# Kernel optimization log

Hardware: AMD Instinct MI355X
Metric: run time of the kernel (lower is better)

Reference implementation:

```python
import jax, jax.numpy as jnp
import numpy as np
import math

FREQ_SEL = [(0, 0), (0, 1), (1, 0), (1, 1)]


def _dct_mat(N):
    # Faithful replica of the module's custom dct1d matrix:
    # A[i, j] = cos(pi * j * (2i + 1) / (2N)) * sqrt(2/N), with row 0 scaled by sqrt(0.5).
    i = np.arange(N, dtype=np.float32)[:, None]
    j = np.arange(N, dtype=np.float32)[None, :]
    A = np.cos(math.pi * j * (2.0 * i + 1.0) / (2.0 * N)) * math.sqrt(2.0 / N)
    A[0] *= math.sqrt(0.5)
    return jnp.asarray(A, dtype=jnp.float32)


def _basis(H, W):
    # coeff(u, v) = sum_{h,w} A_H[u, h] * A_W[v, w] * x[h, w]
    # (both DCT stages in the torch code contract against ROWS of A)
    A_H = _dct_mat(H)
    A_W = _dct_mat(W)
    planes = [A_H[u][:, None] * A_W[v][None, :] for (u, v) in FREQ_SEL]
    return jnp.stack(planes, axis=0)  # [F, H, W]


def setup_inputs() -> dict:
    key = jax.random.key(0)
    k1, k2, k3 = jax.random.split(key, 3)
    B, C, H, W = 32, 256, 64, 64
    hidden = C // 4
    x = jax.random.normal(k1, (B, C, H, W), dtype=jnp.float32)
    w1 = jax.random.normal(k2, (hidden, C), dtype=jnp.float32) * (1.0 / math.sqrt(C))
    w2 = jax.random.normal(k3, (C, hidden), dtype=jnp.float32) * (1.0 / math.sqrt(hidden))
    return {"x": x, "w1": w1, "w2": w2}


def reference(x, w1, w2):
    B, C, H, W = x.shape
    basis = _basis(H, W)                      # [F, H, W]
    spectral = jnp.einsum('bchw,fhw->bcf', x, basis)   # [B, C, F]
    y = jnp.einsum('bcf,hc->bhf', spectral, w1)        # fc1 (1x1 conv1d)
    y = jax.nn.relu(y)
    y = jnp.einsum('bhf,ch->bcf', y, w2)               # fc2
    gate = jax.nn.sigmoid(jnp.mean(y, axis=-1))        # [B, C]
    return x * gate[:, :, None, None]
```

## Files before the change

### kernel.cpp

```cpp
#include <hip/hip_runtime.h>

#define B_  32
#define C_  256
#define HID 64
#define H_  64
#define W_  64
#define HW  4096
#define F_  4

typedef float fvec4 __attribute__((ext_vector_type(4)));

__global__ __launch_bounds__(256) void spectral_kernel(
        const float* __restrict__ x, float* __restrict__ spectral) {
    const int plane = blockIdx.x;
    const int t = threadIdx.x;

    __shared__ float r0[W_], r1[W_];
    if (t < 64) {
        float fh = (float)t;
        r0[t] = cosf(fh * 0.02454369260617026f) * 0.125f;
        r1[t] = cosf(fh * 0.07363107781851077f) * 0.17677669529663689f;
    }
    __syncthreads();

    const float4* xv = (const float4*)(x + (size_t)plane * HW);
    float f0 = 0.f, f1 = 0.f, f2 = 0.f, f3 = 0.f;

    #pragma unroll
    for (int q = 0; q < 4; ++q) {
        int v = q * 256 + t;
        float4 d = xv[v];
        int h  = v >> 4;
        int wb = (v & 15) << 2;
        float r0h = r0[h], r1h = r1[h];
        float e, t0, t1;
        e = d.x; t0 = e * r0[wb+0]; t1 = e * r1[wb+0];
        f0 += r0h*t0; f1 += r0h*t1; f2 += r1h*t0; f3 += r1h*t1;
        e = d.y; t0 = e * r0[wb+1]; t1 = e * r1[wb+1];
        f0 += r0h*t0; f1 += r0h*t1; f2 += r1h*t0; f3 += r1h*t1;
        e = d.z; t0 = e * r0[wb+2]; t1 = e * r1[wb+2];
        f0 += r0h*t0; f1 += r0h*t1; f2 += r1h*t0; f3 += r1h*t1;
        e = d.w; t0 = e * r0[wb+3]; t1 = e * r1[wb+3];
        f0 += r0h*t0; f1 += r0h*t1; f2 += r1h*t0; f3 += r1h*t1;
    }

    #pragma unroll
    for (int off = 32; off >= 1; off >>= 1) {
        f0 += __shfl_down(f0, off);
        f1 += __shfl_down(f1, off);
        f2 += __shfl_down(f2, off);
        f3 += __shfl_down(f3, off);
    }
    __shared__ float part[4][F_];
    int wave = t >> 6, lane = t & 63;
    if (lane == 0) { part[wave][0]=f0; part[wave][1]=f1; part[wave][2]=f2; part[wave][3]=f3; }
    __syncthreads();
    if (t == 0) {
        float4 s;
        s.x = part[0][0]+part[1][0]+part[2][0]+part[3][0];
        s.y = part[0][1]+part[1][1]+part[2][1]+part[3][1];
        s.z = part[0][2]+part[1][2]+part[2][2]+part[3][2];
        s.w = part[0][3]+part[1][3]+part[2][3]+part[3][3];
        ((float4*)spectral)[plane] = s;
    }
}

__global__ __launch_bounds__(256) void gate_kernel(
        const float* __restrict__ spectral, const float* __restrict__ w1,
        const float* __restrict__ w2, float* __restrict__ gate) {
    const int b = blockIdx.x;
    const int t = threadIdx.x;

    __shared__ float s[C_][F_];
    __shared__ float y[HID][F_];

    ((float4*)&s[0][0])[t] = ((const float4*)(spectral + (size_t)b * C_ * F_))[t];
    __syncthreads();

    {
        int h = t >> 2, f = t & 3;
        const float* w1r = w1 + h * C_;
        float a0 = 0.f, a1 = 0.f, a2 = 0.f, a3 = 0.f;
        #pragma unroll 4
        for (int c = 0; c < C_; c += 4) {
            a0 += s[c+0][f] * w1r[c+0];
            a1 += s[c+1][f] * w1r[c+1];
            a2 += s[c+2][f] * w1r[c+2];
            a3 += s[c+3][f] * w1r[c+3];
        }
        y[h][f] = fmaxf((a0 + a1) + (a2 + a3), 0.f);
    }
    __syncthreads();

    {
        int c = t;
        const float* w2r = w2 + c * HID;
        float a0=0.f, a1=0.f, a2=0.f, a3=0.f;
        #pragma unroll 8
        for (int h = 0; h < HID; ++h) {
            float wv = w2r[h];
            a0 += y[h][0]*wv; a1 += y[h][1]*wv; a2 += y[h][2]*wv; a3 += y[h][3]*wv;
        }
        float m = (a0 + a1 + a2 + a3) * 0.25f;
        gate[b * C_ + c] = 1.f / (1.f + __expf(-m) );
    }
}

__global__ __launch_bounds__(256) void scale_kernel(
        const float* __restrict__ x, const float* __restrict__ gate,
        float* __restrict__ out, long long n4) {
    long long i = (long long)blockIdx.x * 256 + threadIdx.x;
    const long long stride = (long long)gridDim.x * 256;
    for (; i < n4; i += stride) {
        fvec4 v = ((const fvec4*)x)[i];
        float g = gate[i >> 10];
        v *= g;
        __builtin_nontemporal_store(v, ((fvec4*)out) + i);
    }
}

extern "C" void kernel_launch(void* const* d_in, const int* in_sizes, int n_in,
                              void* d_out, int out_size, void* d_ws, size_t ws_size,
                              hipStream_t stream) {
    const float* x  = (const float*)d_in[0];
    const float* w1 = (const float*)d_in[1];
    const float* w2 = (const float*)d_in[2];
    float* out = (float*)d_out;

    float* spectral = (float*)d_ws;
    float* gate     = (float*)d_ws + (size_t)B_ * C_ * F_;

    spectral_kernel<<<B_ * C_, 256, 0, stream>>>(x, spectral);
    gate_kernel<<<B_, 256, 0, stream>>>(spectral, w1, w2, gate);

    const long long n4 = (long long)B_ * C_ * HW / 4;
    scale_kernel<<<2048, 256, 0, stream>>>(x, gate, out, n4);
}
```

Measured before the change: 72.87 us.

## Process batch in two chunks so scale pass rereads x from cache

Result: slower. 84.24 us (+15.6%).

```diff
diff --git a/kernel.cpp b/kernel.cpp
--- a/kernel.cpp
+++ b/kernel.cpp
@@ -3,19 +3,18 @@
 #define B_  32
 #define C_  256
 #define HID 64
-#define H_  64
-#define W_  64
 #define HW  4096
 #define F_  4
+#define CHUNK_B 16
 
 typedef float fvec4 __attribute__((ext_vector_type(4)));
 
 __global__ __launch_bounds__(256) void spectral_kernel(
-        const float* __restrict__ x, float* __restrict__ spectral) {
-    const int plane = blockIdx.x;
+        const float* __restrict__ x, float* __restrict__ spectral, int b0) {
+    const int plane = b0 * C_ + blockIdx.x;
     const int t = threadIdx.x;
 
-    __shared__ float r0[W_], r1[W_];
+    __shared__ float r0[64], r1[64];
     if (t < 64) {
         float fh = (float)t;
         r0[t] = cosf(fh * 0.02454369260617026f) * 0.125f;
@@ -23,13 +22,13 @@
     }
     __syncthreads();
 
-    const float4* xv = (const float4*)(x + (size_t)plane * HW);
+    const fvec4* xv = (const fvec4*)x + (size_t)plane * (HW / 4);
     float f0 = 0.f, f1 = 0.f, f2 = 0.f, f3 = 0.f;
 
     #pragma unroll
     for (int q = 0; q < 4; ++q) {
         int v = q * 256 + t;
-        float4 d = xv[v];
+        fvec4 d = xv[v];
         int h  = v >> 4;
         int wb = (v & 15) << 2;
         float r0h = r0[h], r1h = r1[h];
@@ -56,25 +55,25 @@
     if (lane == 0) { part[wave][0]=f0; part[wave][1]=f1; part[wave][2]=f2; part[wave][3]=f3; }
     __syncthreads();
     if (t == 0) {
-        float4 s;
+        fvec4 s;
         s.x = part[0][0]+part[1][0]+part[2][0]+part[3][0];
         s.y = part[0][1]+part[1][1]+part[2][1]+part[3][1];
         s.z = part[0][2]+part[1][2]+part[2][2]+part[3][2];
         s.w = part[0][3]+part[1][3]+part[2][3]+part[3][3];
-        ((float4*)spectral)[plane] = s;
+        ((fvec4*)spectral)[plane] = s;
     }
 }
 
 __global__ __launch_bounds__(256) void gate_kernel(
         const float* __restrict__ spectral, const float* __restrict__ w1,
-        const float* __restrict__ w2, float* __restrict__ gate) {
-    const int b = blockIdx.x;
+        const float* __restrict__ w2, float* __restrict__ gate, int b0) {
+    const int b = b0 + blockIdx.x;
     const int t = threadIdx.x;
 
     __shared__ float s[C_][F_];
     __shared__ float y[HID][F_];
 
-    ((float4*)&s[0][0])[t] = ((const float4*)(spectral + (size_t)b * C_ * F_))[t];
+    ((fvec4*)&s[0][0])[t] = ((const fvec4*)(spectral + (size_t)b * C_ * F_))[t];
     __syncthreads();
 
     {
@@ -93,8 +92,7 @@
     __syncthreads();
 
     {
-        int c = t;
-        const float* w2r = w2 + c * HID;
+        const float* w2r = w2 + t * HID;
         float a0=0.f, a1=0.f, a2=0.f, a3=0.f;
         #pragma unroll 8
         for (int h = 0; h < HID; ++h) {
@@ -102,16 +100,17 @@
             a0 += y[h][0]*wv; a1 += y[h][1]*wv; a2 += y[h][2]*wv; a3 += y[h][3]*wv;
         }
         float m = (a0 + a1 + a2 + a3) * 0.25f;
-        gate[b * C_ + c] = 1.f / (1.f + __expf(-m) );
+        gate[b * C_ + t] = 1.f / (1.f + __expf(-m));
     }
 }
 
 __global__ __launch_bounds__(256) void scale_kernel(
         const float* __restrict__ x, const float* __restrict__ gate,
-        float* __restrict__ out, long long n4) {
-    long long i = (long long)blockIdx.x * 256 + threadIdx.x;
+        float* __restrict__ out, long long start4, long long n4) {
+    long long i = start4 + (long long)blockIdx.x * 256 + threadIdx.x;
+    const long long end = start4 + n4;
     const long long stride = (long long)gridDim.x * 256;
-    for (; i < n4; i += stride) {
+    for (; i < end; i += stride) {
         fvec4 v = ((const fvec4*)x)[i];
         float g = gate[i >> 10];
         v *= g;
@@ -130,9 +129,13 @@
     float* spectral = (float*)d_ws;
     float* gate     = (float*)d_ws + (size_t)B_ * C_ * F_;
 
-    spectral_kernel<<<B_ * C_, 256, 0, stream>>>(x, spectral);
-    gate_kernel<<<B_, 256, 0, stream>>>(spectral, w1, w2, gate);
+    const long long chunk4 = (long long)CHUNK_B * C_ * HW / 4;
 
-    const long long n4 = (long long)B_ * C_ * HW / 4;
-    scale_kernel<<<2048, 256, 0, stream>>>(x, gate, out, n4);
+    for (int chunk = 0; chunk < B_ / CHUNK_B; ++chunk) {
+        const int b0 = chunk * CHUNK_B;
+        spectral_kernel<<<CHUNK_B * C_, 256, 0, stream>>>(x, spectral, b0);
+        gate_kernel<<<CHUNK_B, 256, 0, stream>>>(spectral, w1, w2, gate, b0);
+        scale_kernel<<<2048, 256, 0, stream>>>(x, gate, out,
+                                               (long long)b0 * C_ * HW / 4, chunk4);
+    }
 }
```
